# Kernel optimization log

Hardware: AMD Instinct MI355X
Metric: run time of the kernel (lower is better)

The kernel has to match this reference:

```python
import jax, jax.numpy as jnp
from jax import lax
import numpy as np

B, T, U = 64, 512, 256  # batch, seq_len, num_tags (units)


def setup_inputs() -> dict:
    key = jax.random.key(0)
    k1, k2, k3, k4 = jax.random.split(key, 4)
    potentials = jax.random.normal(k1, (B, T, U), dtype=jnp.float32)
    tags = jax.random.randint(k2, (B, T), 0, U)
    seq_len = jax.random.randint(k3, (B,), 1, T + 1).astype(jnp.int32)
    transitions = jax.random.normal(k4, (U, U), dtype=jnp.float32) * 0.1
    return {"potentials": potentials, "tags": tags, "seq_len": seq_len,
            "transitions": transitions}


def _crf_log_likelihood(potentials, tags, seq_len, transitions):
    """ll = sequence_score - log_norm (standard linear-chain CRF)."""
    Bn, Tn, Un = potentials.shape
    t_idx = jnp.arange(Tn)
    mask = t_idx[None, :] < seq_len[:, None]           # [B,T] valid timesteps

    # --- sequence score: unary + binary (transition) terms ---
    unary = jnp.take_along_axis(potentials, tags[..., None], axis=-1)[..., 0]  # [B,T]
    unary_score = jnp.sum(unary * mask, axis=1)
    trans = transitions[tags[:, :-1], tags[:, 1:]]      # [B,T-1]
    pair_mask = mask[:, 1:]                             # transition t->t+1 valid if t+1 < len
    binary_score = jnp.sum(trans * pair_mask, axis=1)

    # --- log partition via forward algorithm (log-sum-exp semiring scan) ---
    alpha0 = potentials[:, 0]                           # [B,U]

    def step(alpha, xs):
        pot_t, m_t = xs                                 # [B,U], [B]
        # semiring matmul: logsumexp over previous tag
        new = jax.nn.logsumexp(alpha[:, :, None] + transitions[None, :, :], axis=1) + pot_t
        alpha = jnp.where(m_t[:, None], new, alpha)     # freeze finished sequences
        return alpha, None

    xs = (jnp.swapaxes(potentials[:, 1:], 0, 1),        # [T-1,B,U]
          jnp.swapaxes(mask[:, 1:], 0, 1))              # [T-1,B]
    alpha, _ = lax.scan(step, alpha0, xs)
    log_norm = jax.nn.logsumexp(alpha, axis=-1)         # [B]

    return unary_score + binary_score - log_norm


def reference(potentials, tags, seq_len, transitions):
    ll = _crf_log_likelihood(potentials, tags, seq_len, transitions)
    return -jnp.mean(ll)  # train_step loss
```

## Files before the change

kernel.cpp:

```cpp
#include <hip/hip_runtime.h>


#define Bc 64
#define Tc 512
#define Uc 256
#define LOG2E 1.4426950408889634f
#define LN2   0.6931471805599453f
#define CC2   7.2134752f

typedef __bf16 bf16x8 __attribute__((ext_vector_type(8)));
typedef float  f32x4  __attribute__((ext_vector_type(4)));

__device__ __forceinline__ void wg_barrier() {
    asm volatile("s_waitcnt lgkmcnt(0)" ::: "memory");
    __builtin_amdgcn_s_barrier();
    asm volatile("" ::: "memory");
}

__global__ __launch_bounds__(512)
void crf_fwd(const float* __restrict__ pot, const int* __restrict__ tags,
             const int* __restrict__ seqlen, const float* __restrict__ trans,
             float* __restrict__ ws, float* __restrict__ out)
{
    const int b    = blockIdx.x;
    const int tid  = threadIdx.x;
    const int lane = tid & 63;
    const int w    = tid >> 6;
    const int g4   = lane >> 4;
    const int c16  = lane & 15;
    const int L    = seqlen[b];

    __shared__ __align__(16) __bf16 ea_lds[2][Uc];
    __shared__ __align__(16) float mx[2][8];
    __shared__ float wred[8];
    __shared__ float redU[8], redB[8];

    const float* potb = pot  + (size_t)b * Tc * Uc;
    const int*   tagb = tags + b * Tc;

    bf16x8 bfr[8][2];
    #pragma unroll
    for (int kt = 0; kt < 8; ++kt) {
        #pragma unroll
        for (int nt = 0; nt < 2; ++nt) {
            const int u = 32 * w + 16 * nt + c16;
            bf16x8 bb;
            #pragma unroll
            for (int e = 0; e < 8; ++e) {
                const int v = 32 * kt + 8 * g4 + e;
                bb[e] = (__bf16)__builtin_exp2f(trans[v * Uc + u] * LOG2E);
            }
            bfr[kt][nt] = bb;
        }
    }

    {
        const int t  = tid;
        const int tg = tagb[t];
        float up = 0.f, bp = 0.f;
        if (t < L)           up = potb[(size_t)t * Uc + tg];
        if (t >= 1 && t < L) bp = trans[tagb[t - 1] * Uc + tg];
        #pragma unroll
        for (int m = 1; m < 64; m <<= 1) {
            up += __shfl_xor(up, m);
            bp += __shfl_xor(bp, m);
        }
        if (lane == 0) { redU[w] = up; redB[w] = bp; }
    }
    __syncthreads();

    const int um = 32 * w + (lane & 31);

    float pv0 = potb[(size_t)1 * Uc + um];
    float pv1 = potb[(size_t)2 * Uc + um];
    float pv2 = potb[(size_t)3 * Uc + um];
    float pv3 = potb[(size_t)4 * Uc + um];

    float er = __builtin_exp2f(potb[um] * LOG2E);
    float M;
    {
        float m = er;
        m = fmaxf(m, __shfl_xor(m, 1));
        m = fmaxf(m, __shfl_xor(m, 2));
        m = fmaxf(m, __shfl_xor(m, 4));
        m = fmaxf(m, __shfl_xor(m, 8));
        m = fmaxf(m, __shfl_xor(m, 16));
        if (lane == 0) wred[w] = m;
        __syncthreads();
        float g = fmaxf(fmaxf(fmaxf(wred[0], wred[1]), fmaxf(wred[2], wred[3])),
                        fmaxf(fmaxf(wred[4], wred[5]), fmaxf(wred[6], wred[7])));
        const float r = __builtin_amdgcn_rcpf(g);
        M  = -LN2 * __builtin_log2f(r);
        er = er * r;
        if (lane < 32) ea_lds[0][um] = (__bf16)er;
        if (lane == 0) mx[1][w] = m * r;
        __syncthreads();
    }

    #define STEPX(TT, PVC, RP, WP, CHK)                                        \
    {                                                                          \
        bf16x8 af[8];                                                          \
        const __bf16* ebase = &ea_lds[(RP)][8 * g4];                           \
        _Pragma("unroll")                                                      \
        for (int kt = 0; kt < 8; ++kt)                                         \
            af[kt] = *(const bf16x8*)(ebase + 32 * kt);                        \
        float pef = __builtin_exp2f((PVC) * LOG2E - CC2);                      \
        float dM = 0.0f;                                                       \
        const bool dor = (CHK) && (((TT) & 7) == 0);                           \
        if (dor) {                                                             \
            const int sl = ((TT) >> 3) & 1;                                    \
            f32x4 m0 = *(const f32x4*)&mx[sl][0];                              \
            f32x4 m1 = *(const f32x4*)&mx[sl][4];                              \
            float g = fmaxf(fmaxf(fmaxf(m0[0], m0[1]), fmaxf(m0[2], m0[3])),   \
                            fmaxf(fmaxf(m1[0], m1[1]), fmaxf(m1[2], m1[3])));  \
            const float r = __builtin_amdgcn_rcpf(g);                          \
            dM  = -LN2 * __builtin_log2f(r);                                   \
            pef *= r;                                                          \
        }                                                                      \
        const f32x4 z = {0.f, 0.f, 0.f, 0.f};                                  \
        f32x4 c0l = z, c0h = z, c1l = z, c1h = z;                              \
        _Pragma("unroll")                                                      \
        for (int kt = 0; kt < 4; ++kt) {                                       \
            c0l = __builtin_amdgcn_mfma_f32_16x16x32_bf16(af[kt], bfr[kt][0], c0l, 0, 0, 0); \
            c1l = __builtin_amdgcn_mfma_f32_16x16x32_bf16(af[kt], bfr[kt][1], c1l, 0, 0, 0); \
        }                                                                      \
        _Pragma("unroll")                                                      \
        for (int kt = 4; kt < 8; ++kt) {                                       \
            c0h = __builtin_amdgcn_mfma_f32_16x16x32_bf16(af[kt], bfr[kt][0], c0h, 0, 0, 0); \
            c1h = __builtin_amdgcn_mfma_f32_16x16x32_bf16(af[kt], bfr[kt][1], c1h, 0, 0, 0); \
        }                                                                      \
        const float s0 = c0l[0] + c0h[0];                                      \
        const float s1 = c1l[0] + c1h[0];                                      \
        const float sv = (lane & 16) ? s1 : s0;                                \
        er = sv * pef;                                                         \
        if (lane < 32) ea_lds[(WP)][um] = (__bf16)er;                          \
        if (dor) {                                                             \
            M += dM;                                                           \
            float m = er;                                                      \
            m = fmaxf(m, __shfl_xor(m, 1));                                    \
            m = fmaxf(m, __shfl_xor(m, 2));                                    \
            m = fmaxf(m, __shfl_xor(m, 4));                                    \
            m = fmaxf(m, __shfl_xor(m, 8));                                    \
            m = fmaxf(m, __shfl_xor(m, 16));                                   \
            if (lane == 0) mx[(((TT) >> 3) & 1) ^ 1][w] = m;                   \
        }                                                                      \
        wg_barrier();                                                          \
    }

    int t = 1;
    for (; t + 3 < L && t + 7 < Tc; t += 4) {
        {
            const float pvc = pv0;
            pv0 = potb[(size_t)(t + 4) * Uc + um];
            STEPX(t, pvc, (t + 1) & 1, t & 1, 0);
        }
        {
            const float pvc = pv1;
            pv1 = potb[(size_t)(t + 5) * Uc + um];
            STEPX(t + 1, pvc, t & 1, (t + 1) & 1, 0);
        }
        {
            const float pvc = pv2;
            pv2 = potb[(size_t)(t + 6) * Uc + um];
            STEPX(t + 2, pvc, (t + 1) & 1, t & 1, 0);
        }
        {
            const float pvc = pv3;
            pv3 = potb[(size_t)(t + 7) * Uc + um];
            STEPX(t + 3, pvc, t & 1, (t + 1) & 1, 1);
        }
    }
    if (t < L) { STEPX(t, pv0, (t + 1) & 1, t & 1, 1); ++t; }
    if (t < L) { STEPX(t, pv1, (t + 1) & 1, t & 1, 1); ++t; }
    if (t < L) { STEPX(t, pv2, (t + 1) & 1, t & 1, 1); ++t; }
    if (t < L) { STEPX(t, pv3, (t + 1) & 1, t & 1, 1); ++t; }
    for (; t < L; ++t) {
        const float pvc = potb[(size_t)t * Uc + um];
        STEPX(t, pvc, (t + 1) & 1, t & 1, 1);
    }

    {
        float ssum = er;
        ssum += __shfl_xor(ssum, 1);
        ssum += __shfl_xor(ssum, 2);
        ssum += __shfl_xor(ssum, 4);
        ssum += __shfl_xor(ssum, 8);
        ssum += __shfl_xor(ssum, 16);
        if (lane == 0) wred[w] = ssum;
        __syncthreads();
        if (tid == 0) {
            float S = 0.f, uS = 0.f, bS = 0.f;
            #pragma unroll
            for (int i = 0; i < 8; ++i) { S += wred[i]; uS += redU[i]; bS += redB[i]; }
            const float cstep = CC2 * LN2;
            const float logZ = M + (float)(L - 1) * cstep
                             + LN2 * __builtin_log2f(S);
            ws[b] = uS + bS - logZ;
            __threadfence();
            unsigned old = atomicAdd((unsigned*)(ws + Bc), 1u);
            if (old == 0xAAAAAAAAu + (unsigned)(Bc - 1)) {
                __threadfence();
                float S2 = 0.f;
                #pragma unroll
                for (int i = 0; i < Bc; ++i) S2 += ws[i];
                out[0] = -S2 * (1.0f / (float)Bc);
            }
        }
    }
    #undef STEPX
}

extern "C" void kernel_launch(void* const* d_in, const int* in_sizes, int n_in,
                              void* d_out, int out_size, void* d_ws, size_t ws_size,
                              hipStream_t stream) {
    const float* pot   = (const float*)d_in[0];
    const int*   tags  = (const int*)d_in[1];
    const int*   slen  = (const int*)d_in[2];
    const float* trans = (const float*)d_in[3];
    float* wsf = (float*)d_ws;
    float* out = (float*)d_out;

    crf_fwd<<<Bc, 512, 0, stream>>>(pot, tags, slen, trans, wsf, out);
}
```

Before: 290.3 us.

## Split scan step across 16 waves, one 16-column MFMA tile per wave

Doubles the workgroup from 8 to 16 waves. Each wave now owns 16 output tags instead of 32, so every timestep issues half as many MFMAs per wave and keeps half the transition fragments in registers. The aim is to shorten the per-step critical path of this latency-bound sequential scan. The cost is a barrier across twice as many waves each step and wider max and sum reductions across waves.

Result: slower. 316.2 us (+8.9%).

```diff
diff --git a/kernel.cpp b/kernel.cpp
--- a/kernel.cpp
+++ b/kernel.cpp
@@ -4,6 +4,7 @@
 #define Bc 64
 #define Tc 512
 #define Uc 256
+#define NW 16
 #define LOG2E 1.4426950408889634f
 #define LN2   0.6931471805599453f
 #define CC2   7.2134752f
@@ -17,7 +18,7 @@
     asm volatile("" ::: "memory");
 }
 
-__global__ __launch_bounds__(512)
+__global__ __launch_bounds__(1024, 1)
 void crf_fwd(const float* __restrict__ pot, const int* __restrict__ tags,
              const int* __restrict__ seqlen, const float* __restrict__ trans,
              float* __restrict__ ws, float* __restrict__ out)
@@ -31,35 +32,34 @@
     const int L    = seqlen[b];
 
     __shared__ __align__(16) __bf16 ea_lds[2][Uc];
-    __shared__ __align__(16) float mx[2][8];
-    __shared__ float wred[8];
-    __shared__ float redU[8], redB[8];
+    __shared__ __align__(16) float mx[2][NW];
+    __shared__ float wred[NW];
+    __shared__ float redU[NW], redB[NW];
 
     const float* potb = pot  + (size_t)b * Tc * Uc;
     const int*   tagb = tags + b * Tc;
 
-    bf16x8 bfr[8][2];
+    bf16x8 bfr[8];
     #pragma unroll
     for (int kt = 0; kt < 8; ++kt) {
+        const int u = 16 * w + c16;
+        bf16x8 bb;
         #pragma unroll
-        for (int nt = 0; nt < 2; ++nt) {
-            const int u = 32 * w + 16 * nt + c16;
-            bf16x8 bb;
-            #pragma unroll
-            for (int e = 0; e < 8; ++e) {
-                const int v = 32 * kt + 8 * g4 + e;
-                bb[e] = (__bf16)__builtin_exp2f(trans[v * Uc + u] * LOG2E);
-            }
-            bfr[kt][nt] = bb;
-        }
+        for (int e = 0; e < 8; ++e) {
+            const int v = 32 * kt + 8 * g4 + e;
+            bb[e] = (__bf16)__builtin_exp2f(trans[v * Uc + u] * LOG2E);
+        }
+        bfr[kt] = bb;
     }
 
     {
         const int t  = tid;
-        const int tg = tagb[t];
         float up = 0.f, bp = 0.f;
-        if (t < L)           up = potb[(size_t)t * Uc + tg];
-        if (t >= 1 && t < L) bp = trans[tagb[t - 1] * Uc + tg];
+        if (t < L) {
+            const int tg = tagb[t];
+            up = potb[(size_t)t * Uc + tg];
+            if (t >= 1) bp = trans[tagb[t - 1] * Uc + tg];
+        }
         #pragma unroll
         for (int m = 1; m < 64; m <<= 1) {
             up += __shfl_xor(up, m);
@@ -69,7 +69,7 @@
     }
     __syncthreads();
 
-    const int um = 32 * w + (lane & 31);
+    const int um = 16 * w + c16;
 
     float pv0 = potb[(size_t)1 * Uc + um];
     float pv1 = potb[(size_t)2 * Uc + um];
@@ -84,15 +84,21 @@
         m = fmaxf(m, __shfl_xor(m, 2));
         m = fmaxf(m, __shfl_xor(m, 4));
         m = fmaxf(m, __shfl_xor(m, 8));
-        m = fmaxf(m, __shfl_xor(m, 16));
         if (lane == 0) wred[w] = m;
         __syncthreads();
-        float g = fmaxf(fmaxf(fmaxf(wred[0], wred[1]), fmaxf(wred[2], wred[3])),
-                        fmaxf(fmaxf(wred[4], wred[5]), fmaxf(wred[6], wred[7])));
+        f32x4 q0 = *(const f32x4*)&wred[0];
+        f32x4 q1 = *(const f32x4*)&wred[4];
+        f32x4 q2 = *(const f32x4*)&wred[8];
+        f32x4 q3 = *(const f32x4*)&wred[12];
+        float g = fmaxf(
+            fmaxf(fmaxf(fmaxf(q0[0], q0[1]), fmaxf(q0[2], q0[3])),
+                  fmaxf(fmaxf(q1[0], q1[1]), fmaxf(q1[2], q1[3]))),
+            fmaxf(fmaxf(fmaxf(q2[0], q2[1]), fmaxf(q2[2], q2[3])),
+                  fmaxf(fmaxf(q3[0], q3[1]), fmaxf(q3[2], q3[3]))));
         const float r = __builtin_amdgcn_rcpf(g);
         M  = -LN2 * __builtin_log2f(r);
         er = er * r;
-        if (lane < 32) ea_lds[0][um] = (__bf16)er;
+        if (lane < 16) ea_lds[0][um] = (__bf16)er;
         if (lane == 0) mx[1][w] = m * r;
         __syncthreads();
     }
@@ -111,29 +117,27 @@
             const int sl = ((TT) >> 3) & 1;                                    \
             f32x4 m0 = *(const f32x4*)&mx[sl][0];                              \
             f32x4 m1 = *(const f32x4*)&mx[sl][4];                              \
-            float g = fmaxf(fmaxf(fmaxf(m0[0], m0[1]), fmaxf(m0[2], m0[3])),   \
-                            fmaxf(fmaxf(m1[0], m1[1]), fmaxf(m1[2], m1[3])));  \
+            f32x4 m2 = *(const f32x4*)&mx[sl][8];                              \
+            f32x4 m3 = *(const f32x4*)&mx[sl][12];                             \
+            float g = fmaxf(                                                   \
+                fmaxf(fmaxf(fmaxf(m0[0], m0[1]), fmaxf(m0[2], m0[3])),         \
+                      fmaxf(fmaxf(m1[0], m1[1]), fmaxf(m1[2], m1[3]))),        \
+                fmaxf(fmaxf(fmaxf(m2[0], m2[1]), fmaxf(m2[2], m2[3])),         \
+                      fmaxf(fmaxf(m3[0], m3[1]), fmaxf(m3[2], m3[3]))));       \
             const float r = __builtin_amdgcn_rcpf(g);                          \
             dM  = -LN2 * __builtin_log2f(r);                                   \
             pef *= r;                                                          \
         }                                                                      \
         const f32x4 z = {0.f, 0.f, 0.f, 0.f};                                  \
-        f32x4 c0l = z, c0h = z, c1l = z, c1h = z;                              \
+        f32x4 cl = z, ch = z;                                                  \
         _Pragma("unroll")                                                      \
-        for (int kt = 0; kt < 4; ++kt) {                                       \
-            c0l = __builtin_amdgcn_mfma_f32_16x16x32_bf16(af[kt], bfr[kt][0], c0l, 0, 0, 0); \
-            c1l = __builtin_amdgcn_mfma_f32_16x16x32_bf16(af[kt], bfr[kt][1], c1l, 0, 0, 0); \
-        }                                                                      \
+        for (int kt = 0; kt < 4; ++kt)                                         \
+            cl = __builtin_amdgcn_mfma_f32_16x16x32_bf16(af[kt], bfr[kt], cl, 0, 0, 0); \
         _Pragma("unroll")                                                      \
-        for (int kt = 4; kt < 8; ++kt) {                                       \
-            c0h = __builtin_amdgcn_mfma_f32_16x16x32_bf16(af[kt], bfr[kt][0], c0h, 0, 0, 0); \
-            c1h = __builtin_amdgcn_mfma_f32_16x16x32_bf16(af[kt], bfr[kt][1], c1h, 0, 0, 0); \
-        }                                                                      \
-        const float s0 = c0l[0] + c0h[0];                                      \
-        const float s1 = c1l[0] + c1h[0];                                      \
-        const float sv = (lane & 16) ? s1 : s0;                                \
-        er = sv * pef;                                                         \
-        if (lane < 32) ea_lds[(WP)][um] = (__bf16)er;                          \
+        for (int kt = 4; kt < 8; ++kt)                                         \
+            ch = __builtin_amdgcn_mfma_f32_16x16x32_bf16(af[kt], bfr[kt], ch, 0, 0, 0); \
+        er = (cl[0] + ch[0]) * pef;                                            \
+        if (lane < 16) ea_lds[(WP)][um] = (__bf16)er;                          \
         if (dor) {                                                             \
             M += dM;                                                           \
             float m = er;                                                      \
@@ -141,7 +145,6 @@
             m = fmaxf(m, __shfl_xor(m, 2));                                    \
             m = fmaxf(m, __shfl_xor(m, 4));                                    \
             m = fmaxf(m, __shfl_xor(m, 8));                                    \
-            m = fmaxf(m, __shfl_xor(m, 16));                                   \
             if (lane == 0) mx[(((TT) >> 3) & 1) ^ 1][w] = m;                   \
         }                                                                      \
         wg_barrier();                                                          \
@@ -185,13 +188,12 @@
         ssum += __shfl_xor(ssum, 2);
         ssum += __shfl_xor(ssum, 4);
         ssum += __shfl_xor(ssum, 8);
-        ssum += __shfl_xor(ssum, 16);
         if (lane == 0) wred[w] = ssum;
         __syncthreads();
         if (tid == 0) {
             float S = 0.f, uS = 0.f, bS = 0.f;
             #pragma unroll
-            for (int i = 0; i < 8; ++i) { S += wred[i]; uS += redU[i]; bS += redB[i]; }
+            for (int i = 0; i < NW; ++i) { S += wred[i]; uS += redU[i]; bS += redB[i]; }
             const float cstep = CC2 * LN2;
             const float logZ = M + (float)(L - 1) * cstep
                              + LN2 * __builtin_log2f(S);
@@ -220,5 +222,5 @@
     float* wsf = (float*)d_ws;
     float* out = (float*)d_out;
 
-    crf_fwd<<<Bc, 512, 0, stream>>>(pot, tags, slen, trans, wsf, out);
+    crf_fwd<<<Bc, 64 * NW, 0, stream>>>(pot, tags, slen, trans, wsf, out);
 }
```
